# Optimization experiments

Hardware: AMD Instinct MI355X
Metric: run time of the kernel (lower is better)

Reference implementation:

```python
import jax, jax.numpy as jnp
import numpy as np

KH = KW = 3
STRIDE = 1
PAD = 1
DIL = 1
G = 4  # deformable groups


def setup_inputs() -> dict:
    key = jax.random.key(0)
    k1, k2, k3 = jax.random.split(key, 3)
    B, C, H, W = 8, 256, 64, 64
    K = KH * KW
    inp = jax.random.normal(k1, (B, C, H, W), dtype=jnp.float32)
    offset = jax.random.normal(k2, (B, 2 * G * K, H, W), dtype=jnp.float32)
    mask = jax.random.uniform(k3, (B, G * K, H, W), dtype=jnp.float32)
    return {"input": inp, "offset": offset, "mask": mask}


def _deform_sample(x, offset, mask):
    # x: [B,C,H,W]; offset: [B,2*G*K,Ho,Wo]; mask: [B,G*K,Ho,Wo]
    B, C, H, W = x.shape
    K = KH * KW
    Ho = (H + 2 * PAD - DIL * (KH - 1) - 1) // STRIDE + 1
    Wo = (W + 2 * PAD - DIL * (KW - 1) - 1) // STRIDE + 1
    Cg = C // G

    off = offset.reshape(B, G, K, 2, Ho, Wo)  # (dy, dx) per group/tap
    m = mask.reshape(B, G, K, Ho, Wo)

    # base sampling grid per kernel tap
    ky = (jnp.arange(KH) * DIL).repeat(KW)          # [K]
    kx = jnp.tile(jnp.arange(KW) * DIL, KH)          # [K]
    base_y = jnp.arange(Ho) * STRIDE - PAD           # [Ho]
    base_x = jnp.arange(Wo) * STRIDE - PAD           # [Wo]

    # sampling positions [B,G,K,Ho,Wo]
    py = base_y[None, None, None, :, None] + ky[None, None, :, None, None] + off[:, :, :, 0]
    px = base_x[None, None, None, None, :] + kx[None, None, :, None, None] + off[:, :, :, 1]

    y0 = jnp.floor(py).astype(jnp.int32)
    x0 = jnp.floor(px).astype(jnp.int32)
    ly = py - y0.astype(py.dtype)
    lx = px - x0.astype(px.dtype)

    xg = x.reshape(B, G, Cg, H * W)

    def gather(yy, xx, w):
        valid = (yy >= 0) & (yy < H) & (xx >= 0) & (xx < W)
        idx = jnp.clip(yy, 0, H - 1) * W + jnp.clip(xx, 0, W - 1)  # [B,G,K,Ho,Wo]
        g = jnp.take_along_axis(xg, idx.reshape(B, G, 1, -1), axis=3)
        g = g.reshape(B, G, Cg, K, Ho, Wo)
        return g * (w * valid.astype(w.dtype))[:, :, None]

    acc = gather(y0, x0, (1 - ly) * (1 - lx))
    acc = acc + gather(y0, x0 + 1, (1 - ly) * lx)
    acc = acc + gather(y0 + 1, x0, ly * (1 - lx))
    acc = acc + gather(y0 + 1, x0 + 1, ly * lx)

    # mask-weighted accumulation over kernel taps
    out = (acc * m[:, :, None]).sum(axis=3)  # [B,G,Cg,Ho,Wo]
    return out.reshape(B, C, Ho, Wo)


def reference(input, offset, mask):
    return _deform_sample(input, offset, mask)
```

## Files before the change

kernel.cpp:

```cpp
#include <hip/hip_runtime.h>
#include <hip/hip_fp16.h>

#define B_  8
#define C_  256
#define H_  64
#define W_  64
#define G_  4
#define CG_ 64
#define HW_ 4096

#define WROWS 12
#define WCOLS 32
#define SROW  392

typedef _Float16 f16x8 __attribute__((ext_vector_type(8)));
typedef float    f32x4 __attribute__((ext_vector_type(4)));

__global__ __launch_bounds__(256) void to_tiled_f16(const float* __restrict__ in,
                                                    _Float16* __restrict__ out) {
  __shared__ unsigned int tile[64][33];
  const int y = blockIdx.x, g = blockIdx.y, b = blockIdx.z;
  const int tid = threadIdx.x;
  const float* src = in + ((size_t)(b * C_) + g * CG_) * HW_ + y * W_;
  _Float16* dst = out + (size_t)((b * G_ + g) * H_ + y) * (8 * 64 * 8);

  const int ch = tid >> 2;
  const int xh = (tid & 3) * 8;
  const float* sp = src + (size_t)ch * HW_ + xh * 2;
#pragma unroll
  for (int i = 0; i < 4; ++i) {
    const float4 v = *(const float4*)(sp + i * 4);
    const unsigned u0 = ((unsigned)__half_as_ushort(__float2half(v.y)) << 16) |
                        __half_as_ushort(__float2half(v.x));
    const unsigned u1 = ((unsigned)__half_as_ushort(__float2half(v.w)) << 16) |
                        __half_as_ushort(__float2half(v.z));
    tile[ch][xh + i * 2]     = u0;
    tile[ch][xh + i * 2 + 1] = u1;
  }
  __syncthreads();
#pragma unroll
  for (int rr = 0; rr < 2; ++rr) {
    const int r  = tid + rr * 256;
    const int xc = r >> 6, c2 = r & 63;
    uint4 o;
    o.x = tile[c2][xc * 4 + 0];
    o.y = tile[c2][xc * 4 + 1];
    o.z = tile[c2][xc * 4 + 2];
    o.w = tile[c2][xc * 4 + 3];
    *(uint4*)(dst + (size_t)r * 8) = o;
  }
}

struct SM {
  _Float16 S[64][SROW];
  int      escN[64];
  short    escK[64][8];
};

__global__ __launch_bounds__(256, 3) void deform_mfma(const float* __restrict__ x,
                                                      const _Float16* __restrict__ xt,
                                                      const float* __restrict__ off,
                                                      const float* __restrict__ msk,
                                                      float* __restrict__ out) {
  __shared__ SM sm;

  const int orig = blockIdx.x;
  const int wgid = (orig & 7) * 256 + (orig >> 3);
  const int tile = wgid & 63;
  const int bg   = wgid >> 6;
  const int ho0  = (tile >> 2) * 4;
  const int wo0  = (tile & 3) * 16;
  const int b    = bg >> 2;
  const int g    = bg & 3;
  const int tid  = threadIdx.x;

  const int wy0 = min(max(ho0 - 4, 0), H_ - WROWS);
  const int wx0 = min(max(wo0 - 8, 0), W_ - WCOLS);
  const float* slab = x + (size_t)(b * C_ + g * CG_) * HW_;

  {
    float4* z = (float4*)sm.S;
    for (int i = tid; i < 3136; i += 256) z[i] = make_float4(0.f, 0.f, 0.f, 0.f);
  }
  __syncthreads();

  if ((tid & 3) == 0) {
    const int px = tid >> 2;
    const int ho = ho0 + (px >> 4);
    const int wo = wo0 + (px & 15);
    const int pixoff = ho * W_ + wo;

    float dyv[9], dxv[9], mv[9];
#pragma unroll
    for (int k = 0; k < 9; ++k) {
      const size_t obo = (size_t)(b * 72 + (g * 9 + k) * 2) * HW_ + pixoff;
      dyv[k] = off[obo];
      dxv[k] = off[obo + HW_];
      mv[k]  = msk[(size_t)(b * 36 + g * 9 + k) * HW_ + pixoff];
    }

    int en = 0;
#pragma unroll
    for (int k = 0; k < 9; ++k) {
      const int ky = k / 3, kx = k - ky * 3;
      const float py = (float)(ho - 1 + ky) + dyv[k];
      const float qx = (float)(wo - 1 + kx) + dxv[k];
      const float fy = floorf(py), fx = floorf(qx);
      const int y0 = (int)fy, x0 = (int)fx;
      const int y1 = y0 + 1,  x1 = x0 + 1;
      const float ly = py - fy, lx = qx - fx;
      const float m = mv[k];

      const bool vy0 = (unsigned)y0 < (unsigned)H_, vy1 = (unsigned)y1 < (unsigned)H_;
      const bool vx0 = (unsigned)x0 < (unsigned)W_, vx1 = (unsigned)x1 < (unsigned)W_;
      const float w00 = (vy0 && vx0) ? (1.f - ly) * (1.f - lx) * m : 0.f;
      const float w01 = (vy0 && vx1) ? (1.f - ly) * lx * m         : 0.f;
      const float w10 = (vy1 && vx0) ? ly * (1.f - lx) * m         : 0.f;
      const float w11 = (vy1 && vx1) ? ly * lx * m                 : 0.f;

      const int ry0 = y0 - wy0, ry1 = y1 - wy0;
      const int rx0 = x0 - wx0, rx1 = x1 - wx0;
      const bool iy0 = (unsigned)ry0 < WROWS, iy1 = (unsigned)ry1 < WROWS;
      const bool ix0 = (unsigned)rx0 < WCOLS, ix1 = (unsigned)rx1 < WCOLS;
      const bool ok = (w00 == 0.f || (iy0 && ix0)) && (w01 == 0.f || (iy0 && ix1)) &&
                      (w10 == 0.f || (iy1 && ix0)) && (w11 == 0.f || (iy1 && ix1));

      if (ok) {
        const int p00 = (w00 != 0.f) ? ry0 * WCOLS + rx0 : 0;
        const int p01 = (w01 != 0.f) ? ry0 * WCOLS + rx1 : 0;
        const int p10 = (w10 != 0.f) ? ry1 * WCOLS + rx0 : 0;
        const int p11 = (w11 != 0.f) ? ry1 * WCOLS + rx1 : 0;
        sm.S[px][p00] = (_Float16)((float)sm.S[px][p00] + w00);
        sm.S[px][p01] = (_Float16)((float)sm.S[px][p01] + w01);
        sm.S[px][p10] = (_Float16)((float)sm.S[px][p10] + w10);
        sm.S[px][p11] = (_Float16)((float)sm.S[px][p11] + w11);
      } else {
        if (en < 8) sm.escK[px][en] = (short)k;
        ++en;
      }
    }
    sm.escN[px] = min(en, 8);
  }
  __syncthreads();

  const int wv   = tid >> 6;
  const int lane = tid & 63;
  const int arow = lane & 15;
  const int q    = lane >> 4;
  const int prow = wv * 16 + arow;
  const int xc0  = (wx0 >> 3) + q;

  f32x4 acc[4];
#pragma unroll
  for (int mb = 0; mb < 4; ++mb) acc[mb] = (f32x4){0.f, 0.f, 0.f, 0.f};

  const size_t bgh = (size_t)(b * G_ + g) * H_;

#pragma unroll
  for (int kb = 0; kb < WROWS; ++kb) {
    const int y = wy0 + kb;
    const _Float16* xp = xt + (((bgh + y) * 8 + xc0) * 64) * 8 + arow * 8;
    const f16x8 a0 = *(const f16x8*)(xp);
    const f16x8 a1 = *(const f16x8*)(xp + 16 * 8);
    const f16x8 a2 = *(const f16x8*)(xp + 32 * 8);
    const f16x8 a3 = *(const f16x8*)(xp + 48 * 8);
    const f16x8 bf = *(const f16x8*)&sm.S[prow][kb * 32 + q * 8];

    acc[0] = __builtin_amdgcn_mfma_f32_16x16x32_f16(a0, bf, acc[0], 0, 0, 0);
    acc[1] = __builtin_amdgcn_mfma_f32_16x16x32_f16(a1, bf, acc[1], 0, 0, 0);
    acc[2] = __builtin_amdgcn_mfma_f32_16x16x32_f16(a2, bf, acc[2], 0, 0, 0);
    acc[3] = __builtin_amdgcn_mfma_f32_16x16x32_f16(a3, bf, acc[3], 0, 0, 0);
  }

  float* ob = out + (size_t)(b * C_ + g * CG_) * HW_;
  const int colx = arow;
  const int rgrp = q * 4;
  const int px_  = wv * 16 + colx;
  const int ho   = ho0 + wv;
  const int wo   = wo0 + colx;
  const int gofs = ho * W_ + wo;
  const int en   = sm.escN[px_];

#pragma unroll
  for (int mb = 0; mb < 4; ++mb) {
    float c0 = 0.f, c1 = 0.f, c2 = 0.f, c3 = 0.f;
    if (en > 0) {
      const int pixoff = gofs;
      for (int j = 0; j < en; ++j) {
        const int k  = (int)sm.escK[px_][j];
        const int ky = k / 3, kx = k - ky * 3;
        const size_t obo = (size_t)(b * 72 + (g * 9 + k) * 2) * HW_ + pixoff;
        const float dy = off[obo];
        const float dx = off[obo + HW_];
        const float m  = msk[(size_t)(b * 36 + g * 9 + k) * HW_ + pixoff];

        const float py = (float)(ho - 1 + ky) + dy;
        const float qx = (float)(wo - 1 + kx) + dx;
        const float fy = floorf(py), fx = floorf(qx);
        const int y0 = (int)fy, x0 = (int)fx;
        const int y1 = y0 + 1,  x1 = x0 + 1;
        const float ly = py - fy, lx = qx - fx;

        const bool vy0 = (unsigned)y0 < (unsigned)H_, vy1 = (unsigned)y1 < (unsigned)H_;
        const bool vx0 = (unsigned)x0 < (unsigned)W_, vx1 = (unsigned)x1 < (unsigned)W_;
        const float w00 = (vy0 && vx0) ? (1.f - ly) * (1.f - lx) * m : 0.f;
        const float w01 = (vy0 && vx1) ? (1.f - ly) * lx * m         : 0.f;
        const float w10 = (vy1 && vx0) ? ly * (1.f - lx) * m         : 0.f;
        const float w11 = (vy1 && vx1) ? ly * lx * m                 : 0.f;

        const int y0c = min(max(y0, 0), H_ - 1), y1c = min(max(y1, 0), H_ - 1);
        const int x0c = min(max(x0, 0), W_ - 1), x1c = min(max(x1, 0), W_ - 1);
        const int o00 = y0c * W_ + x0c, o01 = y0c * W_ + x1c;
        const int o10 = y1c * W_ + x0c, o11 = y1c * W_ + x1c;

        const float* p0 = slab + (size_t)(mb * 16 + rgrp) * HW_;
        c0 += w00 * p0[o00] + w01 * p0[o01] + w10 * p0[o10] + w11 * p0[o11];
        const float* p1 = p0 + HW_;
        c1 += w00 * p1[o00] + w01 * p1[o01] + w10 * p1[o10] + w11 * p1[o11];
        const float* p2 = p0 + 2 * HW_;
        c2 += w00 * p2[o00] + w01 * p2[o01] + w10 * p2[o10] + w11 * p2[o11];
        const float* p3 = p0 + 3 * HW_;
        c3 += w00 * p3[o00] + w01 * p3[o01] + w10 * p3[o10] + w11 * p3[o11];
      }
    }
    const int chb = mb * 16 + rgrp;
    ob[(size_t)(chb + 0) * HW_ + gofs] = acc[mb][0] + c0;
    ob[(size_t)(chb + 1) * HW_ + gofs] = acc[mb][1] + c1;
    ob[(size_t)(chb + 2) * HW_ + gofs] = acc[mb][2] + c2;
    ob[(size_t)(chb + 3) * HW_ + gofs] = acc[mb][3] + c3;
  }
}

__global__ __launch_bounds__(256) void deform_f32_nchw(const float* __restrict__ x,
                                                       const float* __restrict__ off,
                                                       const float* __restrict__ msk,
                                                       float* __restrict__ out) {
  __shared__ int4   s_o[144];
  __shared__ float4 s_w[144];
  const int woq = blockIdx.x;
  const int ho  = blockIdx.y;
  const int b   = blockIdx.z >> 2;
  const int g   = blockIdx.z & 3;
  const int tid = threadIdx.x;

  if (tid < 144) {
    const int wi = tid / 9, k = tid - wi * 9;
    const int wo = woq * 16 + wi;
    const int ky = k / 3, kx = k - ky * 3;
    const size_t ob = (size_t)(b * 72 + (g * 9 + k) * 2) * HW_ + ho * W_ + wo;
    const float dy = off[ob];
    const float dx = off[ob + HW_];
    const float m  = msk[(size_t)(b * 36 + g * 9 + k) * HW_ + ho * W_ + wo];
    const float py = (float)(ho - 1 + ky) + dy;
    const float px = (float)(wo - 1 + kx) + dx;
    const float fy = floorf(py), fx = floorf(px);
    const int y0 = (int)fy, x0 = (int)fx;
    const int y1 = y0 + 1,  x1 = x0 + 1;
    const float ly = py - fy, lx = px - fx;
    const bool vy0 = (unsigned)y0 < (unsigned)H_, vy1 = (unsigned)y1 < (unsigned)H_;
    const bool vx0 = (unsigned)x0 < (unsigned)W_, vx1 = (unsigned)x1 < (unsigned)W_;
    const float wy0 = (1.f - ly) * m, wy1 = ly * m;
    float4 w;
    w.x = (vy0 && vx0) ? wy0 * (1.f - lx) : 0.f;
    w.y = (vy0 && vx1) ? wy0 * lx         : 0.f;
    w.z = (vy1 && vx0) ? wy1 * (1.f - lx) : 0.f;
    w.w = (vy1 && vx1) ? wy1 * lx         : 0.f;
    const int y0c = min(max(y0, 0), H_ - 1), y1c = min(max(y1, 0), H_ - 1);
    const int x0c = min(max(x0, 0), W_ - 1), x1c = min(max(x1, 0), W_ - 1);
    s_o[tid] = make_int4(y0c * W_ + x0c, y0c * W_ + x1c, y1c * W_ + x0c, y1c * W_ + x1c);
    s_w[tid] = w;
  }
  __syncthreads();

  const int ci = tid & 15, wi = tid >> 4;
  const float* xb = x + (size_t)(b * C_ + g * CG_ + ci * 4) * HW_;
  float a0 = 0.f, a1 = 0.f, a2 = 0.f, a3 = 0.f;
#pragma unroll
  for (int k = 0; k < 9; ++k) {
    const int e = wi * 9 + k;
    const int4   o = s_o[e];
    const float4 w = s_w[e];
    a0 += w.x * xb[o.x] + w.y * xb[o.y] + w.z * xb[o.z] + w.w * xb[o.w];
    const float* x1p = xb + HW_;
    a1 += w.x * x1p[o.x] + w.y * x1p[o.y] + w.z * x1p[o.z] + w.w * x1p[o.w];
    const float* x2p = xb + 2 * HW_;
    a2 += w.x * x2p[o.x] + w.y * x2p[o.y] + w.z * x2p[o.z] + w.w * x2p[o.w];
    const float* x3p = xb + 3 * HW_;
    a3 += w.x * x3p[o.x] + w.y * x3p[o.y] + w.z * x3p[o.z] + w.w * x3p[o.w];
  }
  float* ob = out + (size_t)(b * C_ + g * CG_ + ci * 4) * HW_ + ho * W_ + woq * 16 + wi;
  ob[0] = a0; ob[HW_] = a1; ob[2 * HW_] = a2; ob[3 * HW_] = a3;
}

extern "C" void kernel_launch(void* const* d_in, const int* in_sizes, int n_in,
                              void* d_out, int out_size, void* d_ws, size_t ws_size,
                              hipStream_t stream) {
  const float* inp = (const float*)d_in[0];
  const float* off = (const float*)d_in[1];
  const float* msk = (const float*)d_in[2];
  float* out = (float*)d_out;

  const size_t need = (size_t)B_ * C_ * HW_ * sizeof(_Float16);
  if (ws_size >= need) {
    _Float16* xt = (_Float16*)d_ws;
    to_tiled_f16<<<dim3(H_, G_, B_), 256, 0, stream>>>(inp, xt);
    deform_mfma<<<dim3(2048), 256, 0, stream>>>(inp, xt, off, msk, out);
  } else {
    deform_f32_nchw<<<dim3(4, H_, B_ * G_), 256, 0, stream>>>(inp, off, msk, out);
  }
}
```

Measured before the change: 47.14 us.

## Shrink sampling window, accumulate weights in fp32 LDS atomics, pack K dimension

Result: slower. 112.0 us (+137.7%).

```diff
diff --git a/kernel.cpp b/kernel.cpp
--- a/kernel.cpp
+++ b/kernel.cpp
@@ -9,9 +9,10 @@
 #define CG_ 64
 #define HW_ 4096
 
-#define WROWS 12
-#define WCOLS 32
-#define SROW  392
+#define WROWS 10
+#define WCOLS 24
+#define KPAD  256
+#define SROW  260
 
 typedef _Float16 f16x8 __attribute__((ext_vector_type(8)));
 typedef float    f32x4 __attribute__((ext_vector_type(4)));
@@ -52,12 +53,12 @@
 }
 
 struct SM {
-  _Float16 S[64][SROW];
-  int      escN[64];
-  short    escK[64][8];
+  float S[64][SROW];
+  int   escN[64];
+  short escK[64][10];
 };
 
-__global__ __launch_bounds__(256, 3) void deform_mfma(const float* __restrict__ x,
+__global__ __launch_bounds__(256, 2) void deform_mfma(const float* __restrict__ x,
                                                       const _Float16* __restrict__ xt,
                                                       const float* __restrict__ off,
                                                       const float* __restrict__ msk,
@@ -74,13 +75,14 @@
   const int g    = bg & 3;
   const int tid  = threadIdx.x;
 
-  const int wy0 = min(max(ho0 - 4, 0), H_ - WROWS);
+  const int wy0 = min(max(ho0 - 3, 0), H_ - WROWS);
   const int wx0 = min(max(wo0 - 8, 0), W_ - WCOLS);
   const float* slab = x + (size_t)(b * C_ + g * CG_) * HW_;
 
   {
     float4* z = (float4*)sm.S;
-    for (int i = tid; i < 3136; i += 256) z[i] = make_float4(0.f, 0.f, 0.f, 0.f);
+    for (int i = tid; i < 64 * SROW / 4; i += 256)
+      z[i] = make_float4(0.f, 0.f, 0.f, 0.f);
   }
   __syncthreads();
 
@@ -126,20 +128,16 @@
                       (w10 == 0.f || (iy1 && ix0)) && (w11 == 0.f || (iy1 && ix1));
 
       if (ok) {
-        const int p00 = (w00 != 0.f) ? ry0 * WCOLS + rx0 : 0;
-        const int p01 = (w01 != 0.f) ? ry0 * WCOLS + rx1 : 0;
-        const int p10 = (w10 != 0.f) ? ry1 * WCOLS + rx0 : 0;
-        const int p11 = (w11 != 0.f) ? ry1 * WCOLS + rx1 : 0;
-        sm.S[px][p00] = (_Float16)((float)sm.S[px][p00] + w00);
-        sm.S[px][p01] = (_Float16)((float)sm.S[px][p01] + w01);
-        sm.S[px][p10] = (_Float16)((float)sm.S[px][p10] + w10);
-        sm.S[px][p11] = (_Float16)((float)sm.S[px][p11] + w11);
+        if (w00 != 0.f) atomicAdd(&sm.S[px][ry0 * WCOLS + rx0], w00);
+        if (w01 != 0.f) atomicAdd(&sm.S[px][ry0 * WCOLS + rx1], w01);
+        if (w10 != 0.f) atomicAdd(&sm.S[px][ry1 * WCOLS + rx0], w10);
+        if (w11 != 0.f) atomicAdd(&sm.S[px][ry1 * WCOLS + rx1], w11);
       } else {
-        if (en < 8) sm.escK[px][en] = (short)k;
+        if (en < 10) sm.escK[px][en] = (short)k;
         ++en;
       }
     }
-    sm.escN[px] = min(en, 8);
+    sm.escN[px] = min(en, 10);
   }
   __syncthreads();
 
@@ -148,7 +146,6 @@
   const int arow = lane & 15;
   const int q    = lane >> 4;
   const int prow = wv * 16 + arow;
-  const int xc0  = (wx0 >> 3) + q;
 
   f32x4 acc[4];
 #pragma unroll
@@ -157,14 +154,25 @@
   const size_t bgh = (size_t)(b * G_ + g) * H_;
 
 #pragma unroll
-  for (int kb = 0; kb < WROWS; ++kb) {
-    const int y = wy0 + kb;
-    const _Float16* xp = xt + (((bgh + y) * 8 + xc0) * 64) * 8 + arow * 8;
+  for (int i = 0; i < 8; ++i) {
+    const float4 s0 = *(const float4*)&sm.S[prow][i * 32 + q * 8];
+    const float4 s1 = *(const float4*)&sm.S[prow][i * 32 + q * 8 + 4];
+    f16x8 bf;
+    bf[0] = (_Float16)s0.x; bf[1] = (_Float16)s0.y;
+    bf[2] = (_Float16)s0.z; bf[3] = (_Float16)s0.w;
+    bf[4] = (_Float16)s1.x; bf[5] = (_Float16)s1.y;
+    bf[6] = (_Float16)s1.z; bf[7] = (_Float16)s1.w;
+
+    int chunk = 4 * i + q;
+    int wr = chunk / 3, wc = chunk - wr * 3;
+    if (chunk >= 30) { wr = WROWS - 1; wc = 0; }
+    const int y = wy0 + wr;
+    const int xchunk = (wx0 >> 3) + wc;
+    const _Float16* xp = xt + (((bgh + y) * 8 + xchunk) * 64) * 8 + arow * 8;
     const f16x8 a0 = *(const f16x8*)(xp);
     const f16x8 a1 = *(const f16x8*)(xp + 16 * 8);
     const f16x8 a2 = *(const f16x8*)(xp + 32 * 8);
     const f16x8 a3 = *(const f16x8*)(xp + 48 * 8);
-    const f16x8 bf = *(const f16x8*)&sm.S[prow][kb * 32 + q * 8];
 
     acc[0] = __builtin_amdgcn_mfma_f32_16x16x32_f16(a0, bf, acc[0], 0, 0, 0);
     acc[1] = __builtin_amdgcn_mfma_f32_16x16x32_f16(a1, bf, acc[1], 0, 0, 0);
@@ -185,14 +193,13 @@
   for (int mb = 0; mb < 4; ++mb) {
     float c0 = 0.f, c1 = 0.f, c2 = 0.f, c3 = 0.f;
     if (en > 0) {
-      const int pixoff = gofs;
       for (int j = 0; j < en; ++j) {
         const int k  = (int)sm.escK[px_][j];
         const int ky = k / 3, kx = k - ky * 3;
-        const size_t obo = (size_t)(b * 72 + (g * 9 + k) * 2) * HW_ + pixoff;
+        const size_t obo = (size_t)(b * 72 + (g * 9 + k) * 2) * HW_ + gofs;
         const float dy = off[obo];
         const float dx = off[obo + HW_];
-        const float m  = msk[(size_t)(b * 36 + g * 9 + k) * HW_ + pixoff];
+        const float m  = msk[(size_t)(b * 36 + g * 9 + k) * HW_ + gofs];
 
         const float py = (float)(ho - 1 + ky) + dy;
         const float qx = (float)(wo - 1 + kx) + dx;
```
